# Optimization experiments

Hardware: AMD Instinct MI355X
Metric: run time of the kernel (lower is better)

The kernel has to match this reference:

```python
import jax, jax.numpy as jnp
import numpy as np

N_NODES, N_EDGES, H, Q, RBF = 10000, 160000, 128, 16, 32
CUTOFF_UPPER = 4.5


def tensor_norm(t):
    # Frobenius norm squared over the trailing 3x3 dims -> [n, h]
    return (t * t).sum((-2, -1))


def decompose_tensor(X):
    # X: [n, h, 3, 3] -> I: [n, h] (trace/3), A skew, S symmetric-traceless
    eye = jnp.eye(3, dtype=X.dtype)
    I = jnp.einsum('nhii->nh', X) / 3.0
    Xt = jnp.swapaxes(X, -1, -2)
    A = 0.5 * (X - Xt)
    S = 0.5 * (X + Xt) - I[..., None, None] * eye
    return I, A, S


def I_to_tensor(I):
    return I[..., None, None] * jnp.eye(3, dtype=I.dtype)


def skewtensor_to_vector(A):
    return jnp.stack((A[..., 2, 1], A[..., 0, 2], A[..., 1, 0]), axis=-1)


def vector_to_skewtensor(v):
    z = jnp.zeros_like(v[..., 0])
    rows = jnp.stack((z, -v[..., 2], v[..., 1],
                      v[..., 2], z, -v[..., 0],
                      -v[..., 1], v[..., 0], z), axis=-1)
    return rows.reshape(v.shape[:-1] + (3, 3))


def setup_inputs() -> dict:
    key = jax.random.key(0)
    ks = jax.random.split(key, 12)
    d_in = RBF + 2 * Q  # 64
    inp = {
        'X': jax.random.normal(ks[0], (N_NODES, H, 3, 3), jnp.float32),
        'charges': jax.random.normal(ks[1], (N_NODES, Q), jnp.float32),
        'edge_weight': jax.random.uniform(ks[2], (N_EDGES,), jnp.float32) * CUTOFF_UPPER,
        'edge_attr': jax.random.normal(ks[3], (N_EDGES, RBF), jnp.float32),
        'W1': jax.random.normal(ks[4], (d_in, H), jnp.float32) / np.sqrt(d_in),
        'b1': jnp.zeros((H,), jnp.float32),
        'W2': jax.random.normal(ks[5], (H, 2 * H), jnp.float32) / np.sqrt(H),
        'b2': jnp.zeros((2 * H,), jnp.float32),
        'W3': jax.random.normal(ks[6], (2 * H, 3 * H), jnp.float32) / np.sqrt(2 * H),
        'b3': jnp.zeros((3 * H,), jnp.float32),
        'Wt': jax.random.normal(ks[7], (6, H, H), jnp.float32) / np.sqrt(H),
        'edge_index': jax.random.randint(ks[8], (2, N_EDGES), 0, N_NODES, jnp.int64 if jax.config.jax_enable_x64 else jnp.int32),
    }
    return inp


def reference(X, charges, edge_weight, edge_attr, W1, b1, W2, b2, W3, b3, Wt, edge_index):
    n, h = X.shape[0], X.shape[1]
    src, dst = edge_index[0], edge_index[1]

    # CosineCutoff (cutoff_lower = 0)
    C = 0.5 * (jnp.cos(edge_weight * (jnp.pi / CUTOFF_UPPER)) + 1.0)
    C = C * (edge_weight < CUTOFF_UPPER).astype(X.dtype)

    # edge MLP on [edge_attr | charges_i | charges_j]
    x = jnp.concatenate([edge_attr, charges[src], charges[dst]], axis=-1)
    x = jax.nn.silu(x @ W1 + b1)
    x = jax.nn.silu(x @ W2 + b2)
    x = jax.nn.silu(x @ W3 + b3)
    x = (x * C[:, None]).reshape(-1, 3, h)  # [E, 3, h]

    # normalize node tensor features
    X = X / (tensor_norm(X) + 1.0)[..., None, None]
    I, A, S = decompose_tensor(X)
    I = I @ Wt[0]
    A = jnp.einsum('nhij,hg->ngij', A, Wt[1])
    S = jnp.einsum('nhij,hg->ngij', S, Wt[2])
    Y = A + S + I_to_tensor(I)

    # message passing: gather from dst node, scale by edge factor, scatter-add to src
    Im = jax.ops.segment_sum(x[:, 0, :] * I[dst], src, num_segments=n)
    Av = skewtensor_to_vector(A)
    Am_vec = jax.ops.segment_sum(x[:, 1, :, None] * Av[dst], src, num_segments=n)
    Sm = jax.ops.segment_sum(x[:, 2, :, None, None] * S[dst], src, num_segments=n)
    msg = vector_to_skewtensor(Am_vec) + Sm + I_to_tensor(Im)

    # O(3) recombination
    A2 = jnp.matmul(msg, Y)
    B2 = jnp.matmul(Y, msg)
    I, A, S = decompose_tensor(A2 + B2)

    _X = A + S + I_to_tensor(I)
    normp1 = tensor_norm(_X) + 1.0
    I = I / normp1
    A = A / normp1[..., None, None]
    S = S / normp1[..., None, None]
    I = I @ Wt[3]
    A = jnp.einsum('nhij,hg->ngij', A, Wt[4])
    S = jnp.einsum('nhij,hg->ngij', S, Wt[5])
    dX = A + S + I_to_tensor(I)

    return X + dX + jnp.matmul(dX, dX)
```

## Files before the change

### kernel.cpp

```cpp
#include <hip/hip_runtime.h>
#include <math.h>

#define NND 10000
#define NE  160000
#define HD  128
#define NH  (NND*HD)

typedef _Float16 f16;
typedef _Float16 half8 __attribute__((ext_vector_type(8)));
typedef _Float16 half4 __attribute__((ext_vector_type(4)));
typedef float floatx4 __attribute__((ext_vector_type(4)));

__device__ __forceinline__ float silu_f(float v) {
    return v * (1.0f / (1.0f + __expf(-v)));
}

__global__ __launch_bounds__(256) void w_prep(const float* __restrict__ W1,
                                              const float* __restrict__ W2,
                                              const float* __restrict__ W3,
                                              const float* __restrict__ Wt,
                                              f16* __restrict__ w1t,
                                              f16* __restrict__ w2t,
                                              f16* __restrict__ w3t,
                                              f16* __restrict__ wtT) {
    int id = blockIdx.x * 256 + threadIdx.x;
    if (id < 128*64) { int n = id >> 6, k = id & 63;  w1t[id] = (f16)W1[k*128 + n]; return; }
    id -= 128*64;
    if (id < 256*128) { int n = id >> 7, k = id & 127; w2t[id] = (f16)W2[k*256 + n]; return; }
    id -= 256*128;
    if (id < 384*256) { int n = id >> 8, k = id & 255; w3t[id] = (f16)W3[k*384 + n]; return; }
    id -= 384*256;
    if (id < 6*128*128) {
        int wi = id >> 14, rem = id & 16383;
        int n = rem >> 7, k = rem & 127;
        wtT[(size_t)wi*16384 + n*128 + k] = (f16)Wt[(size_t)wi*16384 + k*128 + n];
    }
}

__global__ __launch_bounds__(256) void hist_kernel(const int* __restrict__ eidx,
                                                   int* __restrict__ hist) {
    int e = blockIdx.x * 256 + threadIdx.x;
    if (e < NE) atomicAdd(&hist[eidx[e]], 1);
}

__global__ __launch_bounds__(1024) void scan_kernel(const int* __restrict__ hist,
                                                    int* __restrict__ offs,
                                                    int* __restrict__ cursor) {
    __shared__ int sums[1024];
    int t = threadIdx.x;
    int base = t * 10;
    int loc[10]; int s = 0;
    #pragma unroll
    for (int i = 0; i < 10; i++) {
        int v = (base + i < NND) ? hist[base + i] : 0;
        loc[i] = s; s += v;
    }
    sums[t] = s;
    __syncthreads();
    for (int off = 1; off < 1024; off <<= 1) {
        int v = (t >= off) ? sums[t - off] : 0;
        __syncthreads();
        sums[t] += v;
        __syncthreads();
    }
    int basesum = (t > 0) ? sums[t - 1] : 0;
    #pragma unroll
    for (int i = 0; i < 10; i++)
        if (base + i < NND) { offs[base + i] = basesum + loc[i]; cursor[base + i] = basesum + loc[i]; }
}

__global__ __launch_bounds__(256) void scatter_kernel(const int* __restrict__ eidx,
                                                      int* __restrict__ cursor,
                                                      int* __restrict__ perm,
                                                      int* __restrict__ ssrc,
                                                      int* __restrict__ sdst) {
    int e = blockIdx.x * 256 + threadIdx.x;
    if (e >= NE) return;
    int s = eidx[e], d = eidx[NE + e];
    int pos = atomicAdd(&cursor[s], 1);
    perm[pos] = e; ssrc[pos] = s; sdst[pos] = d;
}

__global__ __launch_bounds__(256) void node_prep(const float* __restrict__ X,
                                                 f16* __restrict__ comp) {
    int idx = blockIdx.x * 256 + threadIdx.x;
    if (idx >= NH) return;
    const float* xp = X + (size_t)idx * 9;
    float x[9];
    #pragma unroll
    for (int i = 0; i < 9; i++) x[i] = xp[i];
    float nsq = 0.f;
    #pragma unroll
    for (int i = 0; i < 9; i++) nsq = fmaf(x[i], x[i], nsq);
    float inv = 1.0f / (nsq + 1.0f);
    #pragma unroll
    for (int i = 0; i < 9; i++) x[i] *= inv;

    float I0  = (x[0] + x[4] + x[8]) * (1.0f / 3.0f);
    float a0  = 0.5f * (x[7] - x[5]);
    float a1  = 0.5f * (x[2] - x[6]);
    float a2  = 0.5f * (x[3] - x[1]);
    float s00 = x[0] - I0;
    float s11 = x[4] - I0;
    float s22 = x[8] - I0;
    float s01 = 0.5f * (x[1] + x[3]);
    float s02 = 0.5f * (x[2] + x[6]);
    float s12 = 0.5f * (x[5] + x[7]);

    comp[0*NH + idx] = (f16)I0;
    comp[1*NH + idx] = (f16)a0;  comp[2*NH + idx] = (f16)a1;  comp[3*NH + idx] = (f16)a2;
    comp[4*NH + idx] = (f16)s00; comp[5*NH + idx] = (f16)s11; comp[6*NH + idx] = (f16)s22;
    comp[7*NH + idx] = (f16)s01; comp[8*NH + idx] = (f16)s02; comp[9*NH + idx] = (f16)s12;
}

__global__ __launch_bounds__(256) void mix_mfma(const f16* __restrict__ A,
                                                const f16* __restrict__ WtT,
                                                float* __restrict__ C,
                                                f16* __restrict__ Ch,
                                                int w0, int w1, int w2, int writeCh) {
    const int g = blockIdx.y;
    const int baseRow = (g == 0) ? 0   : (g == 1 ? NND   : 4*NND);
    const int Mg      = (g == 0) ? NND : (g == 1 ? 3*NND : 6*NND);
    const int row0 = blockIdx.x * 64;
    if (row0 >= Mg) return;
    const int wi = (g == 0) ? w0 : (g == 1 ? w1 : w2);
    const f16* B = WtT + (size_t)wi * 128 * 128;

    __shared__ f16 As[64 * 136];

    const int t = threadIdx.x;
    const int l = t & 63, wid = t >> 6, lr = l & 15, lh = l >> 4;

    #pragma unroll
    for (int i = 0; i < 4; i++) {
        int id = t + 256 * i;
        int r = id >> 4, ch = id & 15;
        int rr = row0 + r; if (rr >= Mg) rr = Mg - 1;
        *(half8*)&As[r*136 + ch*8] =
            *(const half8*)&A[((size_t)baseRow + rr) * HD + ch*8];
    }
    __syncthreads();

    floatx4 acc[8];
    #pragma unroll
    for (int n = 0; n < 8; n++) acc[n] = (floatx4)0.0f;

    #pragma unroll
    for (int k0 = 0; k0 < 128; k0 += 32) {
        half8 a = *(const half8*)&As[(wid*16 + lr)*136 + k0 + lh*8];
        #pragma unroll
        for (int n = 0; n < 8; n++) {
            half8 b = *(const half8*)&B[(size_t)(n*16 + lr)*128 + k0 + lh*8];
            acc[n] = __builtin_amdgcn_mfma_f32_16x16x32_f16(a, b, acc[n], 0, 0, 0);
        }
    }

    #pragma unroll
    for (int n = 0; n < 8; n++) {
        #pragma unroll
        for (int r = 0; r < 4; r++) {
            int gl = row0 + wid*16 + lh*4 + r;
            if (gl < Mg) {
                size_t grow = (size_t)baseRow + gl;
                int col = n*16 + lr;
                float val = acc[n][r];
                C[grow * HD + col] = val;
                if (writeCh) {
                    int plane = (int)(grow / NND);
                    int node  = (int)(grow - (size_t)plane * NND);
                    Ch[((size_t)node * 10 + plane) * HD + col] = (f16)val;
                }
            }
        }
    }
}

__global__ __launch_bounds__(256, 6) void edge_gemm1(
    const float* __restrict__ edge_attr, const float* __restrict__ charges,
    const int* __restrict__ offs,
    const int* __restrict__ perm, const int* __restrict__ ssrc, const int* __restrict__ sdst,
    const f16* __restrict__ W1t, const float* __restrict__ b1,
    f16* __restrict__ x1b, int n0, int n1)
{
    __shared__ f16 As[64 * 72];
    __shared__ int srcS[64], dstS[64], permS[64];

    const int pbase = offs[n0];
    const int pend  = (n1 >= NND) ? NE : offs[n1];
    const int eb    = blockIdx.x * 64;
    if (pbase + eb >= pend) return;

    const int t = threadIdx.x;
    const int l = t & 63, wid = t >> 6, lr = l & 15, lh = l >> 4;

    if (t < 64) {
        int pe = pbase + eb + t;
        if (pe > NE - 1) pe = NE - 1;
        permS[t] = perm[pe];
        srcS[t]  = ssrc[pe];
        dstS[t]  = sdst[pe];
    }
    __syncthreads();

    {
        int e = t >> 2, q = t & 3;
        #pragma unroll
        for (int jj = 0; jj < 2; jj++) {
            int j = q + jj*4;
            float4 va = *(const float4*)&edge_attr[(size_t)permS[e]*32 + j*4];
            half4 hv; hv[0]=(f16)va.x; hv[1]=(f16)va.y; hv[2]=(f16)va.z; hv[3]=(f16)va.w;
            *(half4*)&As[e*72 + j*4] = hv;
        }
        int node = (q < 2) ? srcS[e] : dstS[e];
        int qq   = (q < 2) ? q : (q - 2);
        int cb   = (q < 2) ? 32 : 48;
        #pragma unroll
        for (int jj = 0; jj < 2; jj++) {
            int j = qq + jj*2;
            float4 vc = *(const float4*)&charges[(size_t)node*16 + j*4];
            half4 hv; hv[0]=(f16)vc.x; hv[1]=(f16)vc.y; hv[2]=(f16)vc.z; hv[3]=(f16)vc.w;
            *(half4*)&As[e*72 + cb + j*4] = hv;
        }
    }
    __syncthreads();

    floatx4 acc[2][4];
    #pragma unroll
    for (int n = 0; n < 2; n++)
        #pragma unroll
        for (int m = 0; m < 4; m++) acc[n][m] = (floatx4)0.0f;

    #pragma unroll
    for (int k0 = 0; k0 < 64; k0 += 32) {
        half8 a[4];
        #pragma unroll
        for (int m = 0; m < 4; m++)
            a[m] = *(const half8*)&As[(m*16 + lr)*72 + k0 + lh*8];
        #pragma unroll
        for (int n = 0; n < 2; n++) {
            half8 b = *(const half8*)&W1t[(size_t)(wid*32 + n*16 + lr)*64 + k0 + lh*8];
            #pragma unroll
            for (int m = 0; m < 4; m++)
                acc[n][m] = __builtin_amdgcn_mfma_f32_16x16x32_f16(a[m], b, acc[n][m], 0, 0, 0);
        }
    }

    #pragma unroll
    for (int n = 0; n < 2; n++) {
        int col = wid*32 + n*16 + lr;
        float bb = b1[col];
        #pragma unroll
        for (int m = 0; m < 4; m++)
            #pragma unroll
            for (int r = 0; r < 4; r++) {
                int e = m*16 + lh*4 + r;
                x1b[(size_t)(eb + e)*128 + col] = (f16)silu_f(acc[n][m][r] + bb);
            }
    }
}

__global__ __launch_bounds__(256, 4) void edge_gemm2(
    const int* __restrict__ offs,
    const f16* __restrict__ x1b,
    const f16* __restrict__ W2t, const float* __restrict__ b2,
    f16* __restrict__ x2b, int n0, int n1)
{
    __shared__ f16 As[64 * 136];

    const int pbase = offs[n0];
    const int pend  = (n1 >= NND) ? NE : offs[n1];
    const int eb    = blockIdx.x * 64;
    if (pbase + eb >= pend) return;

    const int t = threadIdx.x;
    const int l = t & 63, wid = t >> 6, lr = l & 15, lh = l >> 4;

    #pragma unroll
    for (int i = 0; i < 4; i++) {
        int id = t + 256 * i;
        int r = id >> 4, c = id & 15;
        *(half8*)&As[r*136 + c*8] = *(const half8*)&x1b[(size_t)(eb + r)*128 + c*8];
    }
    __syncthreads();

    floatx4 acc[4][4];
    #pragma unroll
    for (int n = 0; n < 4; n++)
        #pragma unroll
        for (int m = 0; m < 4; m++) acc[n][m] = (floatx4)0.0f;

    #pragma unroll
    for (int k0 = 0; k0 < 128; k0 += 32) {
        half8 a[4];
        #pragma unroll
        for (int m = 0; m < 4; m++)
            a[m] = *(const half8*)&As[(m*16 + lr)*136 + k0 + lh*8];
        #pragma unroll
        for (int n = 0; n < 4; n++) {
            half8 b = *(const half8*)&W2t[(size_t)(wid*64 + n*16 + lr)*128 + k0 + lh*8];
            #pragma unroll
            for (int m = 0; m < 4; m++)
                acc[n][m] = __builtin_amdgcn_mfma_f32_16x16x32_f16(a[m], b, acc[n][m], 0, 0, 0);
        }
    }

    #pragma unroll
    for (int n = 0; n < 4; n++) {
        int col = wid*64 + n*16 + lr;
        float bb = b2[col];
        #pragma unroll
        for (int m = 0; m < 4; m++)
            #pragma unroll
            for (int r = 0; r < 4; r++) {
                int e = m*16 + lh*4 + r;
                x2b[(size_t)(eb + e)*256 + col] = (f16)silu_f(acc[n][m][r] + bb);
            }
    }
}

__global__ __launch_bounds__(256, 3) void edge_gemm3(
    const float* __restrict__ edge_weight,
    const int* __restrict__ offs, const int* __restrict__ perm,
    const f16* __restrict__ x2b,
    const f16* __restrict__ W3t, const float* __restrict__ b3,
    f16* __restrict__ vbuf, int n0, int n1)
{
    __shared__ f16 As[64 * 136];
    __shared__ float Cs[64];

    const int pbase = offs[n0];
    const int pend  = (n1 >= NND) ? NE : offs[n1];
    const int eb    = blockIdx.x * 64;
    if (pbase + eb >= pend) return;

    const int t = threadIdx.x;
    const int l = t & 63, wid = t >> 6, lr = l & 15, lh = l >> 4;

    if (t < 64) {
        int pe = pbase + eb + t;
        if (pe > NE - 1) pe = NE - 1;
        float w = edge_weight[perm[pe]];
        float c = 0.5f * (cosf(w * (float)(M_PI / 4.5)) + 1.0f);
        Cs[t] = (w < 4.5f) ? c : 0.0f;
    }

    floatx4 acc[6][4];
    #pragma unroll
    for (int n = 0; n < 6; n++)
        #pragma unroll
        for (int m = 0; m < 4; m++) acc[n][m] = (floatx4)0.0f;

    #pragma unroll
    for (int kb = 0; kb < 2; kb++) {
        __syncthreads();
        #pragma unroll
        for (int i = 0; i < 4; i++) {
            int id = t + 256 * i;
            int r = id >> 4, c = id & 15;
            *(half8*)&As[r*136 + c*8] =
                *(const half8*)&x2b[(size_t)(eb + r)*256 + kb*128 + c*8];
        }
        __syncthreads();

        #pragma unroll
        for (int k0 = 0; k0 < 128; k0 += 32) {
            half8 a[4];
            #pragma unroll
            for (int m = 0; m < 4; m++)
                a[m] = *(const half8*)&As[(m*16 + lr)*136 + k0 + lh*8];
            #pragma unroll
            for (int n = 0; n < 6; n++) {
                half8 b = *(const half8*)&W3t[(size_t)(wid*96 + n*16 + lr)*256 + kb*128 + k0 + lh*8];
                #pragma unroll
                for (int m = 0; m < 4; m++)
                    acc[n][m] = __builtin_amdgcn_mfma_f32_16x16x32_f16(a[m], b, acc[n][m], 0, 0, 0);
            }
        }
    }

    #pragma unroll
    for (int n = 0; n < 6; n++) {
        int col = wid*96 + n*16 + lr;
        float bb = b3[col];
        #pragma unroll
        for (int m = 0; m < 4; m++)
            #pragma unroll
            for (int r = 0; r < 4; r++) {
                int e = m*16 + lh*4 + r;
                vbuf[(size_t)(eb + e)*384 + col] = (f16)(silu_f(acc[n][m][r] + bb) * Cs[e]);
            }
    }
}

__global__ __launch_bounds__(128) void scatter_combine(
    const int* __restrict__ offs, const int* __restrict__ ends,
    const int* __restrict__ sdst, const f16* __restrict__ vbuf,
    const f16* __restrict__ Ych, const float* __restrict__ Yc,
    f16* __restrict__ pre, int n0, int VC)
{
    const int s = n0 + blockIdx.x;
    const int h = threadIdx.x;
    const int pbase = offs[n0];
    const int p0 = offs[s], p1 = ends[s];

    float ps[10];
    #pragma unroll
    for (int c = 0; c < 10; c++) ps[c] = 0.f;

    int p = p0;
    for (; p + 1 < p1; p += 2) {
        int sl0 = p - pbase, sl1 = sl0 + 1;
        int d0 = sdst[p], d1 = sdst[p + 1];
        const f16* y0 = Ych + (size_t)d0 * 1280 + h;
        const f16* y1 = Ych + (size_t)d1 * 1280 + h;
        float va0 = (float)vbuf[(size_t)sl0*384 + h];
        float vb0 = (float)vbuf[(size_t)sl0*384 + 128 + h];
        float vc0 = (float)vbuf[(size_t)sl0*384 + 256 + h];
        float va1 = (float)vbuf[(size_t)sl1*384 + h];
        float vb1 = (float)vbuf[(size_t)sl1*384 + 128 + h];
        float vc1 = (float)vbuf[(size_t)sl1*384 + 256 + h];
        float y0r[10], y1r[10];
        #pragma unroll
        for (int c = 0; c < 10; c++) { y0r[c] = (float)y0[c*HD]; y1r[c] = (float)y1[c*HD]; }
        ps[0] = fmaf(va0, y0r[0], ps[0]);
        #pragma unroll
        for (int c = 1; c < 4; c++)  ps[c] = fmaf(vb0, y0r[c], ps[c]);
        #pragma unroll
        for (int c = 4; c < 10; c++) ps[c] = fmaf(vc0, y0r[c], ps[c]);
        ps[0] = fmaf(va1, y1r[0], ps[0]);
        #pragma unroll
        for (int c = 1; c < 4; c++)  ps[c] = fmaf(vb1, y1r[c], ps[c]);
        #pragma unroll
        for (int c = 4; c < 10; c++) ps[c] = fmaf(vc1, y1r[c], ps[c]);
    }
    if (p < p1) {
        int sl0 = p - pbase;
        int d0 = sdst[p];
        const f16* y0 = Ych + (size_t)d0 * 1280 + h;
        float va0 = (float)vbuf[(size_t)sl0*384 + h];
        float vb0 = (float)vbuf[(size_t)sl0*384 + 128 + h];
        float vc0 = (float)vbuf[(size_t)sl0*384 + 256 + h];
        float y0r[10];
        #pragma unroll
        for (int c = 0; c < 10; c++) y0r[c] = (float)y0[c*HD];
        ps[0] = fmaf(va0, y0r[0], ps[0]);
        #pragma unroll
        for (int c = 1; c < 4; c++)  ps[c] = fmaf(vb0, y0r[c], ps[c]);
        #pragma unroll
        for (int c = 4; c < 10; c++) ps[c] = fmaf(vc0, y0r[c], ps[c]);
    }

    const size_t idx = (size_t)s * HD + h;
    float yI  = Yc[0*(size_t)NH + idx];
    float ya0 = Yc[1*(size_t)NH + idx], ya1 = Yc[2*(size_t)NH + idx], ya2 = Yc[3*(size_t)NH + idx];
    float ys00 = Yc[4*(size_t)NH + idx], ys11 = Yc[5*(size_t)NH + idx], ys22 = Yc[6*(size_t)NH + idx];
    float ys01 = Yc[7*(size_t)NH + idx], ys02 = Yc[8*(size_t)NH + idx], ys12 = Yc[9*(size_t)NH + idx];

    float M[3][3] = {
        { ps[0] + ps[4],  ps[7] - ps[3],  ps[8] + ps[2] },
        { ps[7] + ps[3],  ps[0] + ps[5],  ps[9] - ps[1] },
        { ps[8] - ps[2],  ps[9] + ps[1],  ps[0] + ps[6] } };
    float Y[3][3] = {
        { yI + ys00,  ys01 - ya2, ys02 + ya1 },
        { ys01 + ya2, yI + ys11,  ys12 - ya0 },
        { ys02 - ya1, ys12 + ya0, yI + ys22  } };

    float T[3][3];
    #pragma unroll
    for (int r = 0; r < 3; r++)
        #pragma unroll
        for (int c = 0; c < 3; c++) {
            float acc = 0.f;
            #pragma unroll
            for (int k = 0; k < 3; k++)
                acc += M[r][k] * Y[k][c] + Y[r][k] * M[k][c];
            T[r][c] = acc;
        }

    float tr3 = (T[0][0] + T[1][1] + T[2][2]) * (1.0f / 3.0f);
    float nsq = 0.f;
    #pragma unroll
    for (int r = 0; r < 3; r++)
        #pragma unroll
        for (int c = 0; c < 3; c++) nsq = fmaf(T[r][c], T[r][c], nsq);
    float inv = 1.0f / (nsq + 1.0f);

    pre[0*(size_t)NH + idx] = (f16)(tr3 * inv);
    pre[1*(size_t)NH + idx] = (f16)(0.5f * (T[2][1] - T[1][2]) * inv);
    pre[2*(size_t)NH + idx] = (f16)(0.5f * (T[0][2] - T[2][0]) * inv);
    pre[3*(size_t)NH + idx] = (f16)(0.5f * (T[1][0] - T[0][1]) * inv);
    pre[4*(size_t)NH + idx] = (f16)((T[0][0] - tr3) * inv);
    pre[5*(size_t)NH + idx] = (f16)((T[1][1] - tr3) * inv);
    pre[6*(size_t)NH + idx] = (f16)((T[2][2] - tr3) * inv);
    pre[7*(size_t)NH + idx] = (f16)(0.5f * (T[0][1] + T[1][0]) * inv);
    pre[8*(size_t)NH + idx] = (f16)(0.5f * (T[0][2] + T[2][0]) * inv);
    pre[9*(size_t)NH + idx] = (f16)(0.5f * (T[1][2] + T[2][1]) * inv);
}

__global__ __launch_bounds__(256) void final_out(const float* __restrict__ post,
                                                 const float* __restrict__ X,
                                                 float* __restrict__ out) {
    int idx = blockIdx.x * 256 + threadIdx.x;
    if (idx >= NH) return;

    float dI  = post[0*NH + idx];
    float da0 = post[1*NH + idx], da1 = post[2*NH + idx], da2 = post[3*NH + idx];
    float ds00 = post[4*NH + idx], ds11 = post[5*NH + idx], ds22 = post[6*NH + idx];
    float ds01 = post[7*NH + idx], ds02 = post[8*NH + idx], ds12 = post[9*NH + idx];

    float D[3][3] = {
        { dI + ds00,  ds01 - da2, ds02 + da1 },
        { ds01 + da2, dI + ds11,  ds12 - da0 },
        { ds02 - da1, ds12 + da0, dI + ds22  } };

    const float* xp = X + (size_t)idx * 9;
    float x[9];
    #pragma unroll
    for (int i = 0; i < 9; i++) x[i] = xp[i];
    float nsq = 0.f;
    #pragma unroll
    for (int i = 0; i < 9; i++) nsq = fmaf(x[i], x[i], nsq);
    float inv = 1.0f / (nsq + 1.0f);

    float* op = out + (size_t)idx * 9;
    #pragma unroll
    for (int r = 0; r < 3; r++)
        #pragma unroll
        for (int c = 0; c < 3; c++) {
            float p = 0.f;
            #pragma unroll
            for (int k = 0; k < 3; k++) p = fmaf(D[r][k], D[k][c], p);
            op[r*3 + c] = x[r*3 + c] * inv + D[r][c] + p;
        }
}

extern "C" void kernel_launch(void* const* d_in, const int* in_sizes, int n_in,
                              void* d_out, int out_size, void* d_ws, size_t ws_size,
                              hipStream_t stream) {
    const float* X       = (const float*)d_in[0];
    const float* charges = (const float*)d_in[1];
    const float* ew      = (const float*)d_in[2];
    const float* ea      = (const float*)d_in[3];
    const float* W1      = (const float*)d_in[4];
    const float* b1      = (const float*)d_in[5];
    const float* W2      = (const float*)d_in[6];
    const float* b2      = (const float*)d_in[7];
    const float* W3      = (const float*)d_in[8];
    const float* b3      = (const float*)d_in[9];
    const float* Wt      = (const float*)d_in[10];
    const int*   eidx    = (const int*)d_in[11];
    float* out = (float*)d_out;

    float* f32a  = (float*)d_ws;
    f16*   fh16  = (f16*)(f32a + (size_t)10 * NH);
    f16*   ych   = fh16 + (size_t)10 * NH;
    f16*   w1t   = ych + (size_t)10 * NH;
    f16*   w2t   = w1t + 128*64;
    f16*   w3t   = w2t + 256*128;
    f16*   wtT   = w3t + 384*256;
    int*   hist   = (int*)(wtT + 6*128*128);
    int*   offs   = hist + NND;
    int*   cursor = offs + NND;
    int*   perm   = cursor + NND;
    int*   ssrc   = perm + NE;
    int*   sdst   = ssrc + NE;
    f16*   vbuf   = (f16*)(sdst + NE);

    size_t used = (size_t)((char*)vbuf - (char*)d_ws);
    int Q, VC;
    if      (used + (size_t)160000 * 1536 <= ws_size) { Q = 1; VC = 160000; }
    else if (used + (size_t) 84480 * 1536 <= ws_size) { Q = 2; VC = 84480;  }
    else if (used + (size_t) 48000 * 1536 <= ws_size) { Q = 4; VC = 48000;  }
    else                                              { Q = 8; VC = 24320;  }
    f16* x1b = vbuf + (size_t)VC * 384;
    f16* x2b = x1b  + (size_t)VC * 128;

    hipMemsetAsync(hist, 0, NND * sizeof(int), stream);

    w_prep<<<928, 256, 0, stream>>>(W1, W2, W3, Wt, w1t, w2t, w3t, wtT);
    node_prep<<<NH / 256, 256, 0, stream>>>(X, fh16);

    hist_kernel<<<(NE + 255) / 256, 256, 0, stream>>>(eidx, hist);
    scan_kernel<<<1, 1024, 0, stream>>>(hist, offs, cursor);
    scatter_kernel<<<(NE + 255) / 256, 256, 0, stream>>>(eidx, cursor, perm, ssrc, sdst);

    dim3 gmix((6 * NND + 63) / 64, 3);
    mix_mfma<<<gmix, 256, 0, stream>>>(fh16, wtT, f32a, ych, 0, 1, 2, 1);

    const int nodesPer = NND / Q;
    for (int q = 0; q < Q; q++) {
        int n0 = q * nodesPer, n1 = n0 + nodesPer;
        int nb = VC / 64;
        edge_gemm1<<<nb, 256, 0, stream>>>(ea, charges, offs, perm, ssrc, sdst,
                                           w1t, b1, x1b, n0, n1);
        edge_gemm2<<<nb, 256, 0, stream>>>(offs, x1b, w2t, b2, x2b, n0, n1);
        edge_gemm3<<<nb, 256, 0, stream>>>(ew, offs, perm, x2b, w3t, b3,
                                           vbuf, n0, n1);
        scatter_combine<<<nodesPer, 128, 0, stream>>>(offs, cursor, sdst, vbuf,
                                                      ych, f32a, fh16, n0, VC);
    }

    mix_mfma<<<gmix, 256, 0, stream>>>(fh16, wtT, f32a, ych, 3, 4, 5, 0);

    final_out<<<NH / 256, 256, 0, stream>>>(f32a, X, out);
}
```

Baseline: 460.5 us.

## Fuse edge MLP layers 1 and 2, stage edge outputs via LDS, drop fp32 Y

Merges the first two edge MLP GEMMs into one kernel so the layer-1 activations stay in shared memory instead of round-tripping through global memory. Edge GEMM outputs (x2b, vbuf) are staged in LDS and written back as coalesced 16-byte rows. The first mix pass no longer writes the fp32 Y planes, and scatter_combine reads Y from the fp16 node-interleaved copy instead. This cuts global traffic and one launch, at the cost of more LDS per block (lower occupancy) and Y read at fp16 precision.

```diff
diff --git a/kernel.cpp b/kernel.cpp
--- a/kernel.cpp
+++ b/kernel.cpp
@@ -117,7 +117,8 @@
                                                 const f16* __restrict__ WtT,
                                                 float* __restrict__ C,
                                                 f16* __restrict__ Ch,
-                                                int w0, int w1, int w2, int writeCh) {
+                                                int w0, int w1, int w2,
+                                                int writeC, int writeCh) {
     const int g = blockIdx.y;
     const int baseRow = (g == 0) ? 0   : (g == 1 ? NND   : 4*NND);
     const int Mg      = (g == 0) ? NND : (g == 1 ? 3*NND : 6*NND);
@@ -164,7 +165,7 @@
                 size_t grow = (size_t)baseRow + gl;
                 int col = n*16 + lr;
                 float val = acc[n][r];
-                C[grow * HD + col] = val;
+                if (writeC) C[grow * HD + col] = val;
                 if (writeCh) {
                     int plane = (int)(grow / NND);
                     int node  = (int)(grow - (size_t)plane * NND);
@@ -175,14 +176,18 @@
     }
 }
 
-__global__ __launch_bounds__(256, 6) void edge_gemm1(
+__global__ __launch_bounds__(256, 4) void edge_gemm12(
     const float* __restrict__ edge_attr, const float* __restrict__ charges,
     const int* __restrict__ offs,
     const int* __restrict__ perm, const int* __restrict__ ssrc, const int* __restrict__ sdst,
     const f16* __restrict__ W1t, const float* __restrict__ b1,
-    f16* __restrict__ x1b, int n0, int n1)
+    const f16* __restrict__ W2t, const float* __restrict__ b2,
+    f16* __restrict__ x2b, int n0, int n1)
 {
-    __shared__ f16 As[64 * 72];
+    __shared__ __align__(16) char pool[33280];
+    f16* x0s  = (f16*)pool;
+    f16* x1s  = (f16*)(pool + 9216);
+    f16* x2st = (f16*)pool;
     __shared__ int srcS[64], dstS[64], permS[64];
 
     const int pbase = offs[n0];
@@ -209,7 +214,7 @@
             int j = q + jj*4;
             float4 va = *(const float4*)&edge_attr[(size_t)permS[e]*32 + j*4];
             half4 hv; hv[0]=(f16)va.x; hv[1]=(f16)va.y; hv[2]=(f16)va.z; hv[3]=(f16)va.w;
-            *(half4*)&As[e*72 + j*4] = hv;
+            *(half4*)&x0s[e*72 + j*4] = hv;
         }
         int node = (q < 2) ? srcS[e] : dstS[e];
         int qq   = (q < 2) ? q : (q - 2);
@@ -219,102 +224,85 @@
             int j = qq + jj*2;
             float4 vc = *(const float4*)&charges[(size_t)node*16 + j*4];
             half4 hv; hv[0]=(f16)vc.x; hv[1]=(f16)vc.y; hv[2]=(f16)vc.z; hv[3]=(f16)vc.w;
-            *(half4*)&As[e*72 + cb + j*4] = hv;
-        }
-    }
-    __syncthreads();
-
-    floatx4 acc[2][4];
-    #pragma unroll
-    for (int n = 0; n < 2; n++)
-        #pragma unroll
-        for (int m = 0; m < 4; m++) acc[n][m] = (floatx4)0.0f;
-
-    #pragma unroll
-    for (int k0 = 0; k0 < 64; k0 += 32) {
-        half8 a[4];
-        #pragma unroll
-        for (int m = 0; m < 4; m++)
-            a[m] = *(const half8*)&As[(m*16 + lr)*72 + k0 + lh*8];
+            *(half4*)&x0s[e*72 + cb + j*4] = hv;
+        }
+    }
+    __syncthreads();
+
+    {
+        floatx4 acc[2][4];
+        #pragma unroll
+        for (int n = 0; n < 2; n++)
+            #pragma unroll
+            for (int m = 0; m < 4; m++) acc[n][m] = (floatx4)0.0f;
+
+        #pragma unroll
+        for (int k0 = 0; k0 < 64; k0 += 32) {
+            half8 a[4];
+            #pragma unroll
+            for (int m = 0; m < 4; m++)
+                a[m] = *(const half8*)&x0s[(m*16 + lr)*72 + k0 + lh*8];
+            #pragma unroll
+            for (int n = 0; n < 2; n++) {
+                half8 b = *(const half8*)&W1t[(size_t)(wid*32 + n*16 + lr)*64 + k0 + lh*8];
+                #pragma unroll
+                for (int m = 0; m < 4; m++)
+                    acc[n][m] = __builtin_amdgcn_mfma_f32_16x16x32_f16(a[m], b, acc[n][m], 0, 0, 0);
+            }
+        }
         #pragma unroll
         for (int n = 0; n < 2; n++) {
-            half8 b = *(const half8*)&W1t[(size_t)(wid*32 + n*16 + lr)*64 + k0 + lh*8];
+            int col = wid*32 + n*16 + lr;
+            float bb = b1[col];
             #pragma unroll
             for (int m = 0; m < 4; m++)
-                acc[n][m] = __builtin_amdgcn_mfma_f32_16x16x32_f16(a[m], b, acc[n][m], 0, 0, 0);
-        }
-    }
-
-    #pragma unroll
-    for (int n = 0; n < 2; n++) {
-        int col = wid*32 + n*16 + lr;
-        float bb = b1[col];
-        #pragma unroll
-        for (int m = 0; m < 4; m++)
-            #pragma unroll
-            for (int r = 0; r < 4; r++) {
-                int e = m*16 + lh*4 + r;
-                x1b[(size_t)(eb + e)*128 + col] = (f16)silu_f(acc[n][m][r] + bb);
+                #pragma unroll
+                for (int r = 0; r < 4; r++)
+                    x1s[(m*16 + lh*4 + r)*140 + col] = (f16)silu_f(acc[n][m][r] + bb);
+        }
+    }
+    __syncthreads();
+
+    {
+        floatx4 acc[4][4];
+        #pragma unroll
+        for (int n = 0; n < 4; n++)
+            #pragma unroll
+            for (int m = 0; m < 4; m++) acc[n][m] = (floatx4)0.0f;
+
+        #pragma unroll
+        for (int k0 = 0; k0 < 128; k0 += 32) {
+            half8 a[4];
+            #pragma unroll
+            for (int m = 0; m < 4; m++)
+                a[m] = *(const half8*)&x1s[(m*16 + lr)*140 + k0 + lh*8];
+            #pragma unroll
+            for (int n = 0; n < 4; n++) {
+                half8 b = *(const half8*)&W2t[(size_t)(wid*64 + n*16 + lr)*128 + k0 + lh*8];
+                #pragma unroll
+                for (int m = 0; m < 4; m++)
+                    acc[n][m] = __builtin_amdgcn_mfma_f32_16x16x32_f16(a[m], b, acc[n][m], 0, 0, 0);
             }
-    }
-}
-
-__global__ __launch_bounds__(256, 4) void edge_gemm2(
-    const int* __restrict__ offs,
-    const f16* __restrict__ x1b,
-    const f16* __restrict__ W2t, const float* __restrict__ b2,
-    f16* __restrict__ x2b, int n0, int n1)
-{
-    __shared__ f16 As[64 * 136];
-
-    const int pbase = offs[n0];
-    const int pend  = (n1 >= NND) ? NE : offs[n1];
-    const int eb    = blockIdx.x * 64;
-    if (pbase + eb >= pend) return;
-
-    const int t = threadIdx.x;
-    const int l = t & 63, wid = t >> 6, lr = l & 15, lh = l >> 4;
-
-    #pragma unroll
-    for (int i = 0; i < 4; i++) {
-        int id = t + 256 * i;
-        int r = id >> 4, c = id & 15;
-        *(half8*)&As[r*136 + c*8] = *(const half8*)&x1b[(size_t)(eb + r)*128 + c*8];
-    }
-    __syncthreads();
-
-    floatx4 acc[4][4];
-    #pragma unroll
-    for (int n = 0; n < 4; n++)
-        #pragma unroll
-        for (int m = 0; m < 4; m++) acc[n][m] = (floatx4)0.0f;
-
-    #pragma unroll
-    for (int k0 = 0; k0 < 128; k0 += 32) {
-        half8 a[4];
-        #pragma unroll
-        for (int m = 0; m < 4; m++)
-            a[m] = *(const half8*)&As[(m*16 + lr)*136 + k0 + lh*8];
+        }
+        __syncthreads();
         #pragma unroll
         for (int n = 0; n < 4; n++) {
-            half8 b = *(const half8*)&W2t[(size_t)(wid*64 + n*16 + lr)*128 + k0 + lh*8];
+            int col = wid*64 + n*16 + lr;
+            float bb = b2[col];
             #pragma unroll
             for (int m = 0; m < 4; m++)
-                acc[n][m] = __builtin_amdgcn_mfma_f32_16x16x32_f16(a[m], b, acc[n][m], 0, 0, 0);
-        }
-    }
-
-    #pragma unroll
-    for (int n = 0; n < 4; n++) {
-        int col = wid*64 + n*16 + lr;
-        float bb = b2[col];
-        #pragma unroll
-        for (int m = 0; m < 4; m++)
-            #pragma unroll
-            for (int r = 0; r < 4; r++) {
-                int e = m*16 + lh*4 + r;
-                x2b[(size_t)(eb + e)*256 + col] = (f16)silu_f(acc[n][m][r] + bb);
-            }
+                #pragma unroll
+                for (int r = 0; r < 4; r++)
+                    x2st[(m*16 + lh*4 + r)*260 + col] = (f16)silu_f(acc[n][m][r] + bb);
+        }
+    }
+    __syncthreads();
+
+    #pragma unroll
+    for (int i = 0; i < 8; i++) {
+        int c = t + 256 * i;
+        int e = c >> 5, j = c & 31;
+        *(half8*)&x2b[(size_t)(eb + e)*256 + j*8] = *(const half8*)&x2st[e*260 + j*8];
     }
 }
 
@@ -325,7 +313,9 @@
     const f16* __restrict__ W3t, const float* __restrict__ b3,
     f16* __restrict__ vbuf, int n0, int n1)
 {
-    __shared__ f16 As[64 * 136];
+    __shared__ __align__(16) char pool[49664];
+    f16* As    = (f16*)pool;
+    f16* stage = (f16*)pool;
     __shared__ float Cs[64];
 
     const int pbase = offs[n0];
@@ -377,6 +367,7 @@
             }
         }
     }
+    __syncthreads();
 
     #pragma unroll
     for (int n = 0; n < 6; n++) {
@@ -387,15 +378,23 @@
             #pragma unroll
             for (int r = 0; r < 4; r++) {
                 int e = m*16 + lh*4 + r;
-                vbuf[(size_t)(eb + e)*384 + col] = (f16)(silu_f(acc[n][m][r] + bb) * Cs[e]);
+                stage[e*388 + col] = (f16)(silu_f(acc[n][m][r] + bb) * Cs[e]);
             }
+    }
+    __syncthreads();
+
+    #pragma unroll
+    for (int i = 0; i < 12; i++) {
+        int c = t + 256 * i;
+        int e = c / 48, j = c - e * 48;
+        *(half8*)&vbuf[(size_t)(eb + e)*384 + j*8] = *(const half8*)&stage[e*388 + j*8];
     }
 }
 
 __global__ __launch_bounds__(128) void scatter_combine(
     const int* __restrict__ offs, const int* __restrict__ ends,
     const int* __restrict__ sdst, const f16* __restrict__ vbuf,
-    const f16* __restrict__ Ych, const float* __restrict__ Yc,
+    const f16* __restrict__ Ych,
     f16* __restrict__ pre, int n0, int VC)
 {
     const int s = n0 + blockIdx.x;
@@ -450,11 +449,11 @@
         for (int c = 4; c < 10; c++) ps[c] = fmaf(vc0, y0r[c], ps[c]);
     }
 
-    const size_t idx = (size_t)s * HD + h;
-    float yI  = Yc[0*(size_t)NH + idx];
-    float ya0 = Yc[1*(size_t)NH + idx], ya1 = Yc[2*(size_t)NH + idx], ya2 = Yc[3*(size_t)NH + idx];
-    float ys00 = Yc[4*(size_t)NH + idx], ys11 = Yc[5*(size_t)NH + idx], ys22 = Yc[6*(size_t)NH + idx];
-    float ys01 = Yc[7*(size_t)NH + idx], ys02 = Yc[8*(size_t)NH + idx], ys12 = Yc[9*(size_t)NH + idx];
+    const f16* ys = Ych + (size_t)s * 1280 + h;
+    float yI  = (float)ys[0*HD];
+    float ya0 = (float)ys[1*HD], ya1 = (float)ys[2*HD], ya2 = (float)ys[3*HD];
+    float ys00 = (float)ys[4*HD], ys11 = (float)ys[5*HD], ys22 = (float)ys[6*HD];
+    float ys01 = (float)ys[7*HD], ys02 = (float)ys[8*HD], ys12 = (float)ys[9*HD];
 
     float M[3][3] = {
         { ps[0] + ps[4],  ps[7] - ps[3],  ps[8] + ps[2] },
@@ -485,6 +484,7 @@
         for (int c = 0; c < 3; c++) nsq = fmaf(T[r][c], T[r][c], nsq);
     float inv = 1.0f / (nsq + 1.0f);
 
+    const size_t idx = (size_t)s * HD + h;
     pre[0*(size_t)NH + idx] = (f16)(tr3 * inv);
     pre[1*(size_t)NH + idx] = (f16)(0.5f * (T[2][1] - T[1][2]) * inv);
     pre[2*(size_t)NH + idx] = (f16)(0.5f * (T[0][2] - T[2][0]) * inv);
@@ -568,12 +568,11 @@
 
     size_t used = (size_t)((char*)vbuf - (char*)d_ws);
     int Q, VC;
-    if      (used + (size_t)160000 * 1536 <= ws_size) { Q = 1; VC = 160000; }
-    else if (used + (size_t) 84480 * 1536 <= ws_size) { Q = 2; VC = 84480;  }
-    else if (used + (size_t) 48000 * 1536 <= ws_size) { Q = 4; VC = 48000;  }
+    if      (used + (size_t)160000 * 1280 <= ws_size) { Q = 1; VC = 160000; }
+    else if (used + (size_t) 84480 * 1280 <= ws_size) { Q = 2; VC = 84480;  }
+    else if (used + (size_t) 48000 * 1280 <= ws_size) { Q = 4; VC = 48000;  }
     else                                              { Q = 8; VC = 24320;  }
-    f16* x1b = vbuf + (size_t)VC * 384;
-    f16* x2b = x1b  + (size_t)VC * 128;
+    f16* x2b = vbuf + (size_t)VC * 384;
 
     hipMemsetAsync(hist, 0, NND * sizeof(int), stream);
 
@@ -585,22 +584,21 @@
     scatter_kernel<<<(NE + 255) / 256, 256, 0, stream>>>(eidx, cursor, perm, ssrc, sdst);
 
     dim3 gmix((6 * NND + 63) / 64, 3);
-    mix_mfma<<<gmix, 256, 0, stream>>>(fh16, wtT, f32a, ych, 0, 1, 2, 1);
+    mix_mfma<<<gmix, 256, 0, stream>>>(fh16, wtT, f32a, ych, 0, 1, 2, 0, 1);
 
     const int nodesPer = NND / Q;
     for (int q = 0; q < Q; q++) {
         int n0 = q * nodesPer, n1 = n0 + nodesPer;
         int nb = VC / 64;
-        edge_gemm1<<<nb, 256, 0, stream>>>(ea, charges, offs, perm, ssrc, sdst,
-                                           w1t, b1, x1b, n0, n1);
-        edge_gemm2<<<nb, 256, 0, stream>>>(offs, x1b, w2t, b2, x2b, n0, n1);
+        edge_gemm12<<<nb, 256, 0, stream>>>(ea, charges, offs, perm, ssrc, sdst,
+                                            w1t, b1, w2t, b2, x2b, n0, n1);
         edge_gemm3<<<nb, 256, 0, stream>>>(ew, offs, perm, x2b, w3t, b3,
                                            vbuf, n0, n1);
         scatter_combine<<<nodesPer, 128, 0, stream>>>(offs, cursor, sdst, vbuf,
-                                                      ych, f32a, fh16, n0, VC);
-    }
-
-    mix_mfma<<<gmix, 256, 0, stream>>>(fh16, wtT, f32a, ych, 3, 4, 5, 0);
+                                                      ych, fh16, n0, VC);
+    }
+
+    mix_mfma<<<gmix, 256, 0, stream>>>(fh16, wtT, f32a, ych, 3, 4, 5, 1, 0);
 
     final_out<<<NH / 256, 256, 0, stream>>>(f32a, X, out);
 }
```

Result: faster. 435.7 us (-5.4%).
